# Kernel optimization log

Measured on AMD Instinct MI355X. Metric: run time of the kernel, lower is better.

The kernel has to match this reference:

```python
import jax, jax.numpy as jnp
import numpy as np

NEG = -1e9

def setup_inputs() -> dict:
    key = jax.random.key(0)
    ks = jax.random.split(key, 6)
    B, T, H = 32, 2048, 1024
    dec = jax.random.normal(ks[0], (B, H), dtype=jnp.float32)
    enc = jax.random.normal(ks[1], (B, T, H), dtype=jnp.float32)
    mask = jax.random.randint(ks[2], (B, T), 0, 2).astype(jnp.int32)
    scale = 1.0 / np.sqrt(H)
    W_enc = jax.random.normal(ks[3], (H, H), dtype=jnp.float32) * scale
    W_dec = jax.random.normal(ks[4], (H, H), dtype=jnp.float32) * scale
    v = jax.random.normal(ks[5], (H,), dtype=jnp.float32) * scale
    return {"decoder_hidden": dec, "encoder_outputs": enc, "mask": mask,
            "W_enc": W_enc, "W_dec": W_dec, "v": v}

def reference(decoder_hidden, encoder_outputs, mask, W_enc, W_dec, v):
    # enc proj: [B,T,H] @ W_enc^T ; dec proj: [B,H] @ W_dec^T broadcast over T
    enc_p = jnp.einsum('bth,oh->bto', encoder_outputs, W_enc)
    dec_p = jnp.einsum('bh,oh->bo', decoder_hidden, W_dec)[:, None, :]  # [B,1,H]
    energy = jnp.tanh(enc_p + dec_p)                                    # [B,T,H]
    scores = jnp.einsum('bth,h->bt', energy, v)                         # [B,T]
    scores = jnp.where(mask == 0, NEG, scores)
    attn_weights = jax.nn.softmax(scores, axis=1)                       # [B,T]
    context = jnp.einsum('bt,bth->bh', attn_weights, encoder_outputs)   # [B,H]
    return (context, attn_weights)
```

## Files before the change

kernel.cpp:

```cpp
#include <hip/hip_runtime.h>
#include <hip/hip_bf16.h>
#include <stdint.h>

#define B_ 32
#define T_ 2048
#define H_ 1024
#define M_ (B_*T_)

typedef __bf16 bf16x8 __attribute__((ext_vector_type(8)));
typedef float  f32x4  __attribute__((ext_vector_type(4)));
typedef float  f32x16 __attribute__((ext_vector_type(16)));

__device__ __forceinline__ float tanh_fast(float x) {
    float e = __expf(2.0f * x);
    return 1.0f - 2.0f / (e + 1.0f);
}

__device__ __forceinline__ bf16x8 cvt2(f32x4 f0, f32x4 f1) {
    bf16x8 h;
    h[0] = (__bf16)f0[0]; h[1] = (__bf16)f0[1]; h[2] = (__bf16)f0[2]; h[3] = (__bf16)f0[3];
    h[4] = (__bf16)f1[0]; h[5] = (__bf16)f1[1]; h[6] = (__bf16)f1[2]; h[7] = (__bf16)f1[3];
    return h;
}

__global__ __launch_bounds__(256) void k_prep(const float* __restrict__ We,
                                              __bf16* __restrict__ Wt,
                                              const float* __restrict__ dec,
                                              const float* __restrict__ Wd,
                                              float* __restrict__ decp) {
    int bx = blockIdx.x;
    int tid = threadIdx.x;
    if (bx < 512) {
        int tg = bx * 256 + tid;
        int lane = tg & 63;
        int c = (tg >> 6) & 31;
        int s = tg >> 11;
        int o = c * 32 + (lane & 31);
        int k = s * 16 + (lane >> 5) * 8;
        const f32x4* src = (const f32x4*)&We[(size_t)o * H_ + k];
        *(bf16x8*)&Wt[(size_t)tg * 8] = cvt2(src[0], src[1]);
    } else {
        int bxd = bx - 512;
        int b = bxd & 31, oc = bxd >> 5;
        int o = oc * 64 + (tid >> 2);
        int kq = tid & 3;
        const f32x4* wr = (const f32x4*)&Wd[(size_t)o * H_ + kq * 256];
        const f32x4* dr = (const f32x4*)&dec[(size_t)b * H_ + kq * 256];
        f32x4 s4 = {0.f, 0.f, 0.f, 0.f};
#pragma unroll 8
        for (int i = 0; i < 64; ++i) s4 += wr[i] * dr[i];
        float s = s4[0] + s4[1] + s4[2] + s4[3];
        s += __shfl_xor(s, 1);
        s += __shfl_xor(s, 2);
        if (kq == 0) decp[b * H_ + o] = s;
    }
}

__global__ __launch_bounds__(256, 2) void k_scores(const float* __restrict__ enc,
                                                   const float* __restrict__ decp,
                                                   const __bf16* __restrict__ Wt,
                                                   const float* __restrict__ v,
                                                   float* __restrict__ scores_p) {
    __shared__ __bf16 A_lds[2][64 * 32 * 8];
    __shared__ float red[4][64];

    const int tid = threadIdx.x;
    const int w = tid >> 6, lane = tid & 63;
    const int l5 = lane & 31, q2 = lane >> 5;

    const int bx = blockIdx.x;
    const int xs = bx & 7;
    const int q = bx >> 3;
    const int nt = q & 3;
    const int rg = (q >> 2) * 8 + xs;
    const int m0 = rg * 64;
    const int b = m0 >> 11;
    const int cg0 = nt * 8 + w * 2;

    float dp[2], vvv[2];
#pragma unroll
    for (int ct = 0; ct < 2; ++ct) {
        int col = (cg0 + ct) * 32 + l5;
        dp[ct]  = decp[b * H_ + col];
        vvv[ct] = v[col];
    }

    f32x16 acc[2][2];
#pragma unroll
    for (int rt = 0; rt < 2; ++rt)
#pragma unroll
        for (int ct = 0; ct < 2; ++ct)
#pragma unroll
            for (int g = 0; g < 16; ++g)
                acc[rt][ct][g] = dp[ct];

    const int ko_s = tid & 31;
    const int rbase = (tid >> 5) * 8;
    const float* sbase = &enc[(size_t)(m0 + rbase) * H_ + ko_s * 8];

    {
#pragma unroll
        for (int i = 0; i < 8; ++i) {
            const f32x4* s4 = (const f32x4*)(sbase + (size_t)i * H_);
            int row = rbase + i;
            int cell = row * 32 + ((ko_s & 24) | ((ko_s ^ row) & 7));
            *(bf16x8*)&A_lds[0][cell * 8] = cvt2(s4[0], s4[1]);
        }
    }
    __syncthreads();

    bf16x8 bb[4][2];
#pragma unroll
    for (int p = 0; p < 4; ++p)
#pragma unroll
        for (int ct = 0; ct < 2; ++ct)
            bb[p][ct] = *(const bf16x8*)&Wt[(((size_t)p * 32 + cg0 + ct) * 64 + lane) * 8];

#pragma unroll 1
    for (int kc = 0; kc < 4; ++kc) {
        const __bf16* buf = A_lds[kc & 1];

        f32x4 sr[8][2];
        if (kc < 3) {
            const float* sp0 = sbase + (size_t)(kc + 1) * 256;
#pragma unroll
            for (int i = 0; i < 8; ++i) {
                const f32x4* s4 = (const f32x4*)(sp0 + (size_t)i * H_);
                sr[i][0] = s4[0];
                sr[i][1] = s4[1];
            }
        }

        bf16x8 af[2][2];
#pragma unroll
        for (int p = 0; p < 2; ++p)
#pragma unroll
            for (int rt = 0; rt < 2; ++rt) {
                int row = rt * 32 + l5;
                int ko = p * 2 + q2;
                int cell = row * 32 + ((ko & 24) | ((ko ^ row) & 7));
                af[p][rt] = *(const bf16x8*)&buf[cell * 8];
            }

#pragma unroll
        for (int sl = 0; sl < 16; ++sl) {
            const int s = kc * 16 + sl;
            bf16x8 a0 = af[sl & 1][0], a1 = af[sl & 1][1];
            bf16x8 w0 = bb[s & 3][0],  w1 = bb[s & 3][1];

            {
                int sn = (s + 4) & 63;
#pragma unroll
                for (int ct = 0; ct < 2; ++ct)
                    bb[s & 3][ct] = *(const bf16x8*)&Wt[(((size_t)sn * 32 + cg0 + ct) * 64 + lane) * 8];
            }
            {
                int sl2 = (sl + 2) & 15;
#pragma unroll
                for (int rt = 0; rt < 2; ++rt) {
                    int row = rt * 32 + l5;
                    int ko = sl2 * 2 + q2;
                    int cell = row * 32 + ((ko & 24) | ((ko ^ row) & 7));
                    af[sl & 1][rt] = *(const bf16x8*)&buf[cell * 8];
                }
            }

            acc[0][0] = __builtin_amdgcn_mfma_f32_32x32x16_bf16(a0, w0, acc[0][0], 0, 0, 0);
            acc[0][1] = __builtin_amdgcn_mfma_f32_32x32x16_bf16(a0, w1, acc[0][1], 0, 0, 0);
            acc[1][0] = __builtin_amdgcn_mfma_f32_32x32x16_bf16(a1, w0, acc[1][0], 0, 0, 0);
            acc[1][1] = __builtin_amdgcn_mfma_f32_32x32x16_bf16(a1, w1, acc[1][1], 0, 0, 0);
        }

        if (kc < 3) {
            __bf16* dst = A_lds[(kc + 1) & 1];
#pragma unroll
            for (int i = 0; i < 8; ++i) {
                int row = rbase + i;
                int cell = row * 32 + ((ko_s & 24) | ((ko_s ^ row) & 7));
                *(bf16x8*)&dst[cell * 8] = cvt2(sr[i][0], sr[i][1]);
            }
        }
        __syncthreads();
    }

    float sp[2][16];
#pragma unroll
    for (int rt = 0; rt < 2; ++rt)
#pragma unroll
        for (int g = 0; g < 16; ++g)
            sp[rt][g] = tanh_fast(acc[rt][0][g]) * vvv[0] + tanh_fast(acc[rt][1][g]) * vvv[1];

#pragma unroll
    for (int rt = 0; rt < 2; ++rt)
#pragma unroll
        for (int g = 0; g < 16; ++g) {
            float s = sp[rt][g];
            s += __shfl_xor(s, 1);
            s += __shfl_xor(s, 2);
            s += __shfl_xor(s, 4);
            s += __shfl_xor(s, 8);
            s += __shfl_xor(s, 16);
            sp[rt][g] = s;
        }

    if (l5 == 0) {
#pragma unroll
        for (int rt = 0; rt < 2; ++rt)
#pragma unroll
            for (int g = 0; g < 16; ++g) {
                int row = rt * 32 + (g & 3) + 8 * (g >> 2) + 4 * q2;
                red[w][row] = sp[rt][g];
            }
    }
    __syncthreads();
    if (tid < 64) {
        float s = red[0][tid] + red[1][tid] + red[2][tid] + red[3][tid];
        scores_p[nt * M_ + m0 + tid] = s;
    }
}

__global__ __launch_bounds__(256) void k_softmax(const float* __restrict__ scores_p,
                                                 const int* __restrict__ mask,
                                                 float* __restrict__ attn) {
    int b = blockIdx.x;
    int tid = threadIdx.x;
    int w = tid >> 6, lane = tid & 63;
    __shared__ float sm[2][4];
    float val[8];
    float mx = -3e38f;
#pragma unroll
    for (int ii = 0; ii < 8; ++ii) {
        int idx = b * T_ + tid + ii * 256;
        float s = scores_p[idx] + scores_p[M_ + idx] + scores_p[2 * M_ + idx] + scores_p[3 * M_ + idx];
        s = (mask[idx] == 0) ? -1e9f : s;
        val[ii] = s;
        mx = fmaxf(mx, s);
    }
#pragma unroll
    for (int m = 1; m <= 32; m <<= 1) mx = fmaxf(mx, __shfl_xor(mx, m));
    if (lane == 0) sm[0][w] = mx;
    __syncthreads();
    mx = fmaxf(fmaxf(sm[0][0], sm[0][1]), fmaxf(sm[0][2], sm[0][3]));
    float lsum = 0.f;
#pragma unroll
    for (int ii = 0; ii < 8; ++ii) {
        val[ii] = __expf(val[ii] - mx);
        lsum += val[ii];
    }
#pragma unroll
    for (int m = 1; m <= 32; m <<= 1) lsum += __shfl_xor(lsum, m);
    if (lane == 0) sm[1][w] = lsum;
    __syncthreads();
    float inv = 1.0f / (sm[1][0] + sm[1][1] + sm[1][2] + sm[1][3]);
#pragma unroll
    for (int ii = 0; ii < 8; ++ii)
        attn[b * T_ + tid + ii * 256] = val[ii] * inv;
}

__global__ __launch_bounds__(512) void k_context(const float* __restrict__ enc,
                                                 const float* __restrict__ attn,
                                                 float* __restrict__ ctx) {
    __shared__ f32x4 cred[8][32];
    int bx = blockIdx.x;
    int b = bx >> 3, hc = bx & 7;
    int tid = threadIdx.x;
    int wv = tid >> 6, lane = tid & 63;
    int l5 = lane & 31, tq2 = lane >> 5;
    int h = hc * 128 + l5 * 4;
    const float* ap = &attn[b * T_ + wv * 256 + tq2];
    const float* ep = &enc[((size_t)b * T_ + wv * 256 + tq2) * H_ + h];
    f32x4 acc = {0.f, 0.f, 0.f, 0.f};
#pragma unroll 8
    for (int i = 0; i < 128; ++i) {
        float a = ap[2 * i];
        f32x4 e = *(const f32x4*)(ep + (size_t)2 * i * H_);
        acc += a * e;
    }
#pragma unroll
    for (int c = 0; c < 4; ++c) acc[c] += __shfl_xor(acc[c], 32);
    if (tq2 == 0) cred[wv][l5] = acc;
    __syncthreads();
    if (tid < 32) {
        f32x4 r = cred[0][tid];
#pragma unroll
        for (int j = 1; j < 8; ++j) r += cred[j][tid];
        *(f32x4*)&ctx[b * H_ + hc * 128 + tid * 4] = r;
    }
}

extern "C" void kernel_launch(void* const* d_in, const int* in_sizes, int n_in,
                              void* d_out, int out_size, void* d_ws, size_t ws_size,
                              hipStream_t stream) {
    (void)in_sizes; (void)n_in; (void)out_size; (void)ws_size;
    const float* dec  = (const float*)d_in[0];
    const float* enc  = (const float*)d_in[1];
    const int*   mask = (const int*)d_in[2];
    const float* We   = (const float*)d_in[3];
    const float* Wd   = (const float*)d_in[4];
    const float* v    = (const float*)d_in[5];

    float* out = (float*)d_out;
    char* ws = (char*)d_ws;
    float*  decp     = (float*)ws;
    float*  scores_p = (float*)(ws + 131072);
    __bf16* Wt       = (__bf16*)(ws + 131072 + 1048576);

    k_prep   <<<1024, 256, 0, stream>>>(We, Wt, dec, Wd, decp);
    k_scores <<<4096, 256, 0, stream>>>(enc, decp, Wt, v, scores_p);
    k_softmax<<<32, 256, 0, stream>>>(scores_p, mask, out + B_ * H_);
    k_context<<<256, 512, 0, stream>>>(enc, out + B_ * H_, out);
}
```

Before: 581.5 us.

## Single-buffer scores LDS for higher occupancy and split context reduction across T

The scores kernel drops LDS double-buffering and shrinks the register prefetch depth for the weight fragments, and launch bounds go from 2 to 4 blocks per SM. The aim is to hide latency through more resident waves rather than explicit software pipelining, at the cost of an extra barrier per K chunk. The context kernel now splits T into 32 segments across 1024 blocks. It writes partial sums to workspace, which a new reduction kernel adds up, exposing more parallelism for the bandwidth-bound pass over the encoder outputs. The partial-sum buffer reuses the scores workspace region, which is safe only because softmax has already consumed it.

```diff
diff --git a/kernel.cpp b/kernel.cpp
--- a/kernel.cpp
+++ b/kernel.cpp
@@ -56,12 +56,12 @@
     }
 }
 
-__global__ __launch_bounds__(256, 2) void k_scores(const float* __restrict__ enc,
+__global__ __launch_bounds__(256, 4) void k_scores(const float* __restrict__ enc,
                                                    const float* __restrict__ decp,
                                                    const __bf16* __restrict__ Wt,
                                                    const float* __restrict__ v,
                                                    float* __restrict__ scores_p) {
-    __shared__ __bf16 A_lds[2][64 * 32 * 8];
+    __shared__ __bf16 A_lds[64 * 32 * 8];
     __shared__ float red[4][64];
 
     const int tid = threadIdx.x;
@@ -104,33 +104,21 @@
             const f32x4* s4 = (const f32x4*)(sbase + (size_t)i * H_);
             int row = rbase + i;
             int cell = row * 32 + ((ko_s & 24) | ((ko_s ^ row) & 7));
-            *(bf16x8*)&A_lds[0][cell * 8] = cvt2(s4[0], s4[1]);
+            *(bf16x8*)&A_lds[cell * 8] = cvt2(s4[0], s4[1]);
         }
     }
-    __syncthreads();
-
-    bf16x8 bb[4][2];
-#pragma unroll
-    for (int p = 0; p < 4; ++p)
+
+    bf16x8 bb[2][2];
+#pragma unroll
+    for (int p = 0; p < 2; ++p)
 #pragma unroll
         for (int ct = 0; ct < 2; ++ct)
             bb[p][ct] = *(const bf16x8*)&Wt[(((size_t)p * 32 + cg0 + ct) * 64 + lane) * 8];
 
+    __syncthreads();
+
 #pragma unroll 1
     for (int kc = 0; kc < 4; ++kc) {
-        const __bf16* buf = A_lds[kc & 1];
-
-        f32x4 sr[8][2];
-        if (kc < 3) {
-            const float* sp0 = sbase + (size_t)(kc + 1) * 256;
-#pragma unroll
-            for (int i = 0; i < 8; ++i) {
-                const f32x4* s4 = (const f32x4*)(sp0 + (size_t)i * H_);
-                sr[i][0] = s4[0];
-                sr[i][1] = s4[1];
-            }
-        }
-
         bf16x8 af[2][2];
 #pragma unroll
         for (int p = 0; p < 2; ++p)
@@ -139,29 +127,29 @@
                 int row = rt * 32 + l5;
                 int ko = p * 2 + q2;
                 int cell = row * 32 + ((ko & 24) | ((ko ^ row) & 7));
-                af[p][rt] = *(const bf16x8*)&buf[cell * 8];
+                af[p][rt] = *(const bf16x8*)&A_lds[cell * 8];
             }
 
 #pragma unroll
         for (int sl = 0; sl < 16; ++sl) {
             const int s = kc * 16 + sl;
             bf16x8 a0 = af[sl & 1][0], a1 = af[sl & 1][1];
-            bf16x8 w0 = bb[s & 3][0],  w1 = bb[s & 3][1];
+            bf16x8 w0 = bb[s & 1][0],  w1 = bb[s & 1][1];
 
             {
-                int sn = (s + 4) & 63;
+                int sn = (s + 2) & 63;
 #pragma unroll
                 for (int ct = 0; ct < 2; ++ct)
-                    bb[s & 3][ct] = *(const bf16x8*)&Wt[(((size_t)sn * 32 + cg0 + ct) * 64 + lane) * 8];
-            }
-            {
-                int sl2 = (sl + 2) & 15;
+                    bb[s & 1][ct] = *(const bf16x8*)&Wt[(((size_t)sn * 32 + cg0 + ct) * 64 + lane) * 8];
+            }
+            if (sl < 14) {
+                int sl2 = sl + 2;
 #pragma unroll
                 for (int rt = 0; rt < 2; ++rt) {
                     int row = rt * 32 + l5;
                     int ko = sl2 * 2 + q2;
                     int cell = row * 32 + ((ko & 24) | ((ko ^ row) & 7));
-                    af[sl & 1][rt] = *(const bf16x8*)&buf[cell * 8];
+                    af[sl & 1][rt] = *(const bf16x8*)&A_lds[cell * 8];
                 }
             }
 
@@ -172,15 +160,22 @@
         }
 
         if (kc < 3) {
-            __bf16* dst = A_lds[(kc + 1) & 1];
+            bf16x8 st[8];
+            const float* sp0 = sbase + (size_t)(kc + 1) * 256;
+#pragma unroll
+            for (int i = 0; i < 8; ++i) {
+                const f32x4* s4 = (const f32x4*)(sp0 + (size_t)i * H_);
+                st[i] = cvt2(s4[0], s4[1]);
+            }
+            __syncthreads();
 #pragma unroll
             for (int i = 0; i < 8; ++i) {
                 int row = rbase + i;
                 int cell = row * 32 + ((ko_s & 24) | ((ko_s ^ row) & 7));
-                *(bf16x8*)&dst[cell * 8] = cvt2(sr[i][0], sr[i][1]);
-            }
+                *(bf16x8*)&A_lds[cell * 8] = st[i];
+            }
+            __syncthreads();
         }
-        __syncthreads();
     }
 
     float sp[2][16];
@@ -203,6 +198,7 @@
             sp[rt][g] = s;
         }
 
+    __syncthreads();
     if (l5 == 0) {
 #pragma unroll
         for (int rt = 0; rt < 2; ++rt)
@@ -257,35 +253,31 @@
         attn[b * T_ + tid + ii * 256] = val[ii] * inv;
 }
 
-__global__ __launch_bounds__(512) void k_context(const float* __restrict__ enc,
+__global__ __launch_bounds__(256) void k_context(const float* __restrict__ enc,
                                                  const float* __restrict__ attn,
-                                                 float* __restrict__ ctx) {
-    __shared__ f32x4 cred[8][32];
+                                                 float* __restrict__ ctxp) {
     int bx = blockIdx.x;
-    int b = bx >> 3, hc = bx & 7;
-    int tid = threadIdx.x;
-    int wv = tid >> 6, lane = tid & 63;
-    int l5 = lane & 31, tq2 = lane >> 5;
-    int h = hc * 128 + l5 * 4;
-    const float* ap = &attn[b * T_ + wv * 256 + tq2];
-    const float* ep = &enc[((size_t)b * T_ + wv * 256 + tq2) * H_ + h];
+    int b = bx >> 5, seg = bx & 31;
+    int t0 = seg * 64;
+    const float* ep = &enc[((size_t)b * T_ + t0) * H_ + threadIdx.x * 4];
+    const float* ap = &attn[b * T_ + t0];
     f32x4 acc = {0.f, 0.f, 0.f, 0.f};
 #pragma unroll 8
-    for (int i = 0; i < 128; ++i) {
-        float a = ap[2 * i];
-        f32x4 e = *(const f32x4*)(ep + (size_t)2 * i * H_);
-        acc += a * e;
-    }
-#pragma unroll
-    for (int c = 0; c < 4; ++c) acc[c] += __shfl_xor(acc[c], 32);
-    if (tq2 == 0) cred[wv][l5] = acc;
-    __syncthreads();
-    if (tid < 32) {
-        f32x4 r = cred[0][tid];
-#pragma unroll
-        for (int j = 1; j < 8; ++j) r += cred[j][tid];
-        *(f32x4*)&ctx[b * H_ + hc * 128 + tid * 4] = r;
-    }
+    for (int t = 0; t < 64; ++t) {
+        float a = ap[t];
+        acc += a * *(const f32x4*)(ep + (size_t)t * H_);
+    }
+    *(f32x4*)&ctxp[((size_t)seg * B_ + b) * H_ + threadIdx.x * 4] = acc;
+}
+
+__global__ __launch_bounds__(256) void k_ctxred(const float* __restrict__ ctxp,
+                                                float* __restrict__ ctx) {
+    int i = blockIdx.x * 256 + threadIdx.x;
+    float s = 0.f;
+#pragma unroll
+    for (int sg = 0; sg < 32; ++sg)
+        s += ctxp[(size_t)sg * (B_ * H_) + i];
+    ctx[i] = s;
 }
 
 extern "C" void kernel_launch(void* const* d_in, const int* in_sizes, int n_in,
@@ -304,9 +296,11 @@
     float*  decp     = (float*)ws;
     float*  scores_p = (float*)(ws + 131072);
     __bf16* Wt       = (__bf16*)(ws + 131072 + 1048576);
+    float*  ctxp     = (float*)(ws + 131072);
 
     k_prep   <<<1024, 256, 0, stream>>>(We, Wt, dec, Wd, decp);
     k_scores <<<4096, 256, 0, stream>>>(enc, decp, Wt, v, scores_p);
     k_softmax<<<32, 256, 0, stream>>>(scores_p, mask, out + B_ * H_);
-    k_context<<<256, 512, 0, stream>>>(enc, out + B_ * H_, out);
-}
+    k_context<<<1024, 256, 0, stream>>>(enc, out + B_ * H_, ctxp);
+    k_ctxred <<<128, 256, 0, stream>>>(ctxp, out);
+}
```

Result: slower. 710.9 us (+22.2%).
